# Kernel optimization log

Hardware: AMD Instinct MI355X
Metric: run time of the kernel (lower is better)

## Reference

```python
import jax, jax.numpy as jnp
import numpy as np

B, S, D, H = 1, 4096, 1024, 16
HD = D // H  # 64


def setup_inputs() -> dict:
    key = jax.random.key(0)
    k1, k2, k3, k4, k5 = jax.random.split(key, 5)
    hidden_states = jax.random.normal(k1, (B, S, D), dtype=jnp.float32)
    # rotary frequencies: freqs_cis[s, j] = exp(i * s * theta^(-2j/HD)), stored as (cos, sin)
    inv_freq = 1.0 / (10000.0 ** (jnp.arange(0, HD, 2, dtype=jnp.float32) / HD))  # [HD/2]
    angles = jnp.arange(S, dtype=jnp.float32)[:, None] * inv_freq[None, :]        # [S, HD/2]
    freqs_cis = jnp.stack([jnp.cos(angles), jnp.sin(angles)], axis=-1)            # [S, HD/2, 2]
    attention_mask = jnp.ones((B, S), dtype=jnp.float32)
    scale = 1.0 / np.sqrt(D)
    wq = jax.random.normal(k2, (D, D), dtype=jnp.float32) * scale
    wk = jax.random.normal(k3, (D, D), dtype=jnp.float32) * scale
    wv = jax.random.normal(k4, (D, D), dtype=jnp.float32) * scale
    wo = jax.random.normal(k5, (D, D), dtype=jnp.float32) * scale
    return {"hidden_states": hidden_states, "freqs_cis": freqs_cis,
            "attention_mask": attention_mask, "wq": wq, "wk": wk, "wv": wv, "wo": wo}


def _apply_rope(x, freqs_cis):
    # x: [B, S, H, HD]; freqs_cis: [S, HD/2, 2] (cos, sin)
    b, s, h, hd = x.shape
    xr = x.reshape(b, s, h, hd // 2, 2)
    a, bb = xr[..., 0], xr[..., 1]
    cos = freqs_cis[None, :s, None, :, 0]
    sin = freqs_cis[None, :s, None, :, 1]
    out_r = a * cos - bb * sin
    out_i = a * sin + bb * cos
    return jnp.stack([out_r, out_i], axis=-1).reshape(b, s, h, hd)


def reference(hidden_states, freqs_cis, attention_mask, wq, wk, wv, wo):
    b, s, d = hidden_states.shape
    scaling = HD ** -0.5
    q = (hidden_states @ wq).reshape(b, s, H, HD)
    k = (hidden_states @ wk).reshape(b, s, H, HD)
    v = (hidden_states @ wv).reshape(b, s, H, HD)
    q = _apply_rope(q, freqs_cis)
    k = _apply_rope(k, freqs_cis)
    # [B, H, S, S] scores, exactly as the torch module materializes them
    scores = jnp.einsum('bqhd,bkhd->bhqk', q, k) * scaling
    mask_add = (1.0 - attention_mask)[:, None, None, :] * -10000.0  # [B,1,1,S]
    scores = scores + mask_add
    attn = jax.nn.softmax(scores.astype(jnp.float32), axis=-1).astype(q.dtype)
    out = jnp.einsum('bhqk,bkhd->bqhd', attn, v).reshape(b, s, d)
    return out @ wo
```

## Files before the change

### kernel.cpp

```cpp
#include <hip/hip_runtime.h>
#include <stdint.h>

#define S_LEN 4096
#define DMODEL 1024
#define NH 16
#define HDIM 64
#define LOG2E 1.44269504088896340736f

typedef __attribute__((ext_vector_type(8))) __bf16 bf16x8;
typedef __attribute__((ext_vector_type(4))) __bf16 bf16x4;
typedef __attribute__((ext_vector_type(2))) __bf16 bf16x2;
typedef __attribute__((ext_vector_type(4))) float f32x4;
typedef __attribute__((ext_vector_type(16))) float f32x16;
typedef __attribute__((ext_vector_type(4))) unsigned int uint32x4;

__device__ __forceinline__ void gload_lds16(const __bf16* g, __bf16* l) {
  __builtin_amdgcn_global_load_lds(
      (const __attribute__((address_space(1))) void*)g,
      (__attribute__((address_space(3))) void*)l, 16, 0, 0);
}

__global__ __launch_bounds__(256) void convert_f32_bf16(const float* __restrict__ src,
                                                        __bf16* __restrict__ dst,
                                                        const float* __restrict__ mask,
                                                        float* __restrict__ maskadd) {
  int idx = blockIdx.x * 256 + threadIdx.x;
  f32x4 v = ((const f32x4*)src)[idx];
  bf16x4 o;
#pragma unroll
  for (int i = 0; i < 4; ++i) o[i] = (__bf16)v[i];
  ((bf16x4*)dst)[idx] = o;
  if (idx < S_LEN) maskadd[idx] = (1.0f - mask[idx]) * (-10000.0f * LOG2E);
}

template <typename T>
__global__ __launch_bounds__(256) void transpose_tiles(const T* __restrict__ src,
                                                       __bf16* __restrict__ dst,
                                                       int R, int C) {
  src += (size_t)blockIdx.z * R * C;
  dst += (size_t)blockIdx.z * R * C;
  __shared__ __bf16 tile[64][65];
  const int r0 = blockIdx.y * 64, c0 = blockIdx.x * 64;
  const int t = threadIdx.x;
  const int col = t & 63, rsub = t >> 6;
#pragma unroll
  for (int i = 0; i < 16; ++i) {
    int r = rsub + i * 4;
    tile[r][col] = (__bf16)src[(size_t)(r0 + r) * C + (c0 + col)];
  }
  __syncthreads();
#pragma unroll
  for (int i = 0; i < 16; ++i) {
    int r = rsub + i * 4;
    dst[(size_t)(c0 + r) * R + (r0 + col)] = tile[col][r];
  }
}

template <int EPI>
__global__ __launch_bounds__(256) void gemm_bt(const __bf16* __restrict__ A,
                                               const __bf16* __restrict__ BT,
                                               __bf16* __restrict__ Cq,
                                               __bf16* __restrict__ Ck,
                                               __bf16* __restrict__ Cv,
                                               float* __restrict__ Cout,
                                               int Kdim, int Ndim) {
  __shared__ __align__(16) __bf16 At[128][32];
  __shared__ __align__(16) __bf16 Bt[128][32];
  const int t = threadIdx.x;
  const int wave = t >> 6, lane = t & 63;
  const int wr = wave >> 1, wc = wave & 1;
  const int lrow = lane & 15, lk = lane >> 4;
  const int bm = blockIdx.x, bn = blockIdx.y;

  f32x4 acc[4][4];
#pragma unroll
  for (int i = 0; i < 4; ++i)
#pragma unroll
    for (int j = 0; j < 4; ++j) acc[i][j] = f32x4{0.f, 0.f, 0.f, 0.f};

  const int arow0 = bm * 128, brow0 = bn * 128;
  const int srow = wave * 16 + (lane >> 2);
  const int scol = (lane & 3) * 8;
  const __bf16* gA0 = &A[(size_t)(arow0 + srow) * Kdim + scol];
  const __bf16* gA1 = &A[(size_t)(arow0 + 64 + srow) * Kdim + scol];
  const __bf16* gB0 = &BT[(size_t)(brow0 + srow) * Kdim + scol];
  const __bf16* gB1 = &BT[(size_t)(brow0 + 64 + srow) * Kdim + scol];
  __bf16* lA0 = &At[wave * 16][0];
  __bf16* lA1 = &At[64 + wave * 16][0];
  __bf16* lB0 = &Bt[wave * 16][0];
  __bf16* lB1 = &Bt[64 + wave * 16][0];

  for (int k0 = 0; k0 < Kdim; k0 += 32) {
    __syncthreads();
    gload_lds16(gA0 + k0, lA0);
    gload_lds16(gA1 + k0, lA1);
    gload_lds16(gB0 + k0, lB0);
    gload_lds16(gB1 + k0, lB1);
    __syncthreads();
    bf16x8 af[4], bfr[4];
#pragma unroll
    for (int mi = 0; mi < 4; ++mi)
      af[mi] = *(const bf16x8*)&At[wr * 64 + mi * 16 + lrow][lk * 8];
#pragma unroll
    for (int ni = 0; ni < 4; ++ni)
      bfr[ni] = *(const bf16x8*)&Bt[wc * 64 + ni * 16 + lrow][lk * 8];
#pragma unroll
    for (int mi = 0; mi < 4; ++mi)
#pragma unroll
      for (int ni = 0; ni < 4; ++ni)
        acc[mi][ni] =
            __builtin_amdgcn_mfma_f32_16x16x32_bf16(af[mi], bfr[ni], acc[mi][ni], 0, 0, 0);
  }

  const int rb = bm * 128 + wr * 64 + lk * 4;
  const int cb = bn * 128 + wc * 64 + lrow;
#pragma unroll
  for (int mi = 0; mi < 4; ++mi)
#pragma unroll
    for (int ni = 0; ni < 4; ++ni) {
      int c = cb + ni * 16;
#pragma unroll
      for (int r = 0; r < 4; ++r) {
        int row = rb + mi * 16 + r;
        float v = acc[mi][ni][r];
        if (EPI == 0) {
          Cout[(size_t)row * Ndim + c] = v;
        } else {
          int type = c >> 10, d = c & 1023;
          int hh = d >> 6, hd = d & 63;
          __bf16* dp = (type == 0) ? Cq : (type == 1) ? Ck : Cv;
          dp[((size_t)hh * S_LEN + row) * HDIM + hd] = (__bf16)v;
        }
      }
    }
}

__global__ __launch_bounds__(256) void rope_kernel(__bf16* __restrict__ Q,
                                                   __bf16* __restrict__ Kb,
                                                   const float* __restrict__ freqs) {
  size_t idx = (size_t)blockIdx.x * 256 + threadIdx.x;
  int i = idx & 31;
  size_t rest = idx >> 5;
  int s = rest & 4095;
  int h = (int)(rest >> 12);
  float c = freqs[(s * 32 + i) * 2 + 0];
  float sn = freqs[(s * 32 + i) * 2 + 1];
  size_t base = ((size_t)h * S_LEN + s) * HDIM + 2 * i;
  float qa = (float)Q[base], qb = (float)Q[base + 1];
  Q[base] = (__bf16)(qa * c - qb * sn);
  Q[base + 1] = (__bf16)(qa * sn + qb * c);
  float ka = (float)Kb[base], kb2 = (float)Kb[base + 1];
  Kb[base] = (__bf16)(ka * c - kb2 * sn);
  Kb[base + 1] = (__bf16)(ka * sn + kb2 * c);
}

template <int KS>
__global__ __launch_bounds__(256, 2) void attn_split(const __bf16* __restrict__ Q,
                                                     const __bf16* __restrict__ Kmat,
                                                     const __bf16* __restrict__ Vt,
                                                     const float* __restrict__ maskadd,
                                                     float* __restrict__ Opart,
                                                     float* __restrict__ Lpart) {
  constexpr int KCHUNK = S_LEN / KS;
  __shared__ __align__(16) __bf16 Kl[2][64][64];
  __shared__ __align__(16) __bf16 Vl[2][64][64];

  const int t = threadIdx.x;
  const int id = blockIdx.x;
  const int swz = (id & 7) * (16 * NH * KS / 8) + (id >> 3);
  const int h = swz / (16 * KS);
  const int rem = swz % (16 * KS);
  const int qb = rem / KS;
  const int split = rem % KS;
  const int k0 = split * KCHUNK;
  const int wave = t >> 6, lane = t & 63;
  const int lq = lane & 31, hi = lane >> 5;
  const int sw = lq & 7;

  const __bf16* Kh = Kmat + (size_t)h * S_LEN * HDIM;
  const __bf16* Vh = Vt + (size_t)h * HDIM * S_LEN;

  const int sr = t >> 2;
  const int sc0 = (t & 3) * 2;
  const int scs0 = (sc0 ^ (sr & 7)) * 8;
  const int scs1 = ((sc0 + 1) ^ (sr & 7)) * 8;
  const __bf16* Kgb = Kh + (size_t)sr * HDIM + sc0 * 8;
  const __bf16* Vgb = Vh + (size_t)sr * S_LEN + sc0 * 8;

  uint32x4 kreg0, kreg1, vreg0, vreg1;
  kreg0 = *(const uint32x4*)(Kgb + (size_t)k0 * HDIM);
  kreg1 = *(const uint32x4*)(Kgb + (size_t)k0 * HDIM + 8);
  vreg0 = *(const uint32x4*)(Vgb + k0);
  vreg1 = *(const uint32x4*)(Vgb + k0 + 8);
  *(uint32x4*)&Kl[0][sr][scs0] = kreg0;
  *(uint32x4*)&Kl[0][sr][scs1] = kreg1;
  *(uint32x4*)&Vl[0][sr][scs0] = vreg0;
  *(uint32x4*)&Vl[0][sr][scs1] = vreg1;

  const __bf16* Qh = Q + ((size_t)h * S_LEN + qb * 256 + wave * 64 + lq) * HDIM;
  bf16x8 qfA[4], qfB[4];
#pragma unroll
  for (int ds = 0; ds < 4; ++ds) {
    qfA[ds] = *(const bf16x8*)(Qh + ds * 16 + hi * 8);
    qfB[ds] = *(const bf16x8*)(Qh + (size_t)32 * HDIM + ds * 16 + hi * 8);
  }

  __syncthreads();

  const float SCL = 0.125f * LOG2E;
  float lA = 0.f, lB = 0.f;
  f32x16 oA0, oA1, oB0, oB1;
#pragma unroll
  for (int r = 0; r < 16; ++r) { oA0[r] = 0.f; oA1[r] = 0.f; oB0[r] = 0.f; oB1[r] = 0.f; }

  for (int it = 0; it < KCHUNK / 64; ++it) {
    const int cur = it & 1;
    const int kb = k0 + it * 64;

    if (it < KCHUNK / 64 - 1) {
      kreg0 = *(const uint32x4*)(Kgb + (size_t)(kb + 64) * HDIM);
      kreg1 = *(const uint32x4*)(Kgb + (size_t)(kb + 64) * HDIM + 8);
      vreg0 = *(const uint32x4*)(Vgb + (kb + 64));
      vreg1 = *(const uint32x4*)(Vgb + (kb + 64) + 8);
    }

    f32x16 pA0, pA1, pB0, pB1;
#pragma unroll
    for (int r = 0; r < 16; ++r) { pA0[r] = 0.f; pA1[r] = 0.f; pB0[r] = 0.f; pB1[r] = 0.f; }
    __builtin_amdgcn_s_setprio(1);
#pragma unroll
    for (int ds = 0; ds < 4; ++ds) {
      int sg = ((ds << 1) | hi) ^ sw;
      bf16x8 kf0 = *(const bf16x8*)&Kl[cur][lq][sg * 8];
      pA0 = __builtin_amdgcn_mfma_f32_32x32x16_bf16(kf0, qfA[ds], pA0, 0, 0, 0);
      pB0 = __builtin_amdgcn_mfma_f32_32x32x16_bf16(kf0, qfB[ds], pB0, 0, 0, 0);
    }
#pragma unroll
    for (int ds = 0; ds < 4; ++ds) {
      int sg = ((ds << 1) | hi) ^ sw;
      bf16x8 kf1 = *(const bf16x8*)&Kl[cur][lq + 32][sg * 8];
      pA1 = __builtin_amdgcn_mfma_f32_32x32x16_bf16(kf1, qfA[ds], pA1, 0, 0, 0);
      pB1 = __builtin_amdgcn_mfma_f32_32x32x16_bf16(kf1, qfB[ds], pB1, 0, 0, 0);
    }
    __builtin_amdgcn_s_setprio(0);

#pragma unroll
    for (int tq = 0; tq < 4; ++tq) {
      f32x4 ma0 = *(const f32x4*)&maskadd[kb + tq * 8 + hi * 4];
      f32x4 ma1 = *(const f32x4*)&maskadd[kb + 32 + tq * 8 + hi * 4];
#pragma unroll
      for (int c = 0; c < 4; ++c) {
        pA0[tq * 4 + c] = exp2f(fmaf(pA0[tq * 4 + c], SCL, ma0[c]));
        pB0[tq * 4 + c] = exp2f(fmaf(pB0[tq * 4 + c], SCL, ma0[c]));
        pA1[tq * 4 + c] = exp2f(fmaf(pA1[tq * 4 + c], SCL, ma1[c]));
        pB1[tq * 4 + c] = exp2f(fmaf(pB1[tq * 4 + c], SCL, ma1[c]));
      }
    }
    {
      float a0 = (pA0[0] + pA0[1]) + (pA0[2] + pA0[3]);
      float a1 = (pA0[4] + pA0[5]) + (pA0[6] + pA0[7]);
      float a2 = (pA0[8] + pA0[9]) + (pA0[10] + pA0[11]);
      float a3 = (pA0[12] + pA0[13]) + (pA0[14] + pA0[15]);
      float b0 = (pA1[0] + pA1[1]) + (pA1[2] + pA1[3]);
      float b1 = (pA1[4] + pA1[5]) + (pA1[6] + pA1[7]);
      float b2 = (pA1[8] + pA1[9]) + (pA1[10] + pA1[11]);
      float b3 = (pA1[12] + pA1[13]) + (pA1[14] + pA1[15]);
      float ps = ((a0 + a1) + (a2 + a3)) + ((b0 + b1) + (b2 + b3));
      ps += __shfl_xor(ps, 32);
      lA += ps;
    }
    {
      float a0 = (pB0[0] + pB0[1]) + (pB0[2] + pB0[3]);
      float a1 = (pB0[4] + pB0[5]) + (pB0[6] + pB0[7]);
      float a2 = (pB0[8] + pB0[9]) + (pB0[10] + pB0[11]);
      float a3 = (pB0[12] + pB0[13]) + (pB0[14] + pB0[15]);
      float b0 = (pB1[0] + pB1[1]) + (pB1[2] + pB1[3]);
      float b1 = (pB1[4] + pB1[5]) + (pB1[6] + pB1[7]);
      float b2 = (pB1[8] + pB1[9]) + (pB1[10] + pB1[11]);
      float b3 = (pB1[12] + pB1[13]) + (pB1[14] + pB1[15]);
      float ps = ((a0 + a1) + (a2 + a3)) + ((b0 + b1) + (b2 + b3));
      ps += __shfl_xor(ps, 32);
      lB += ps;
    }

    unsigned int tA0[8], tA1[8], tB0[8], tB1[8];
#pragma unroll
    for (int tp = 0; tp < 8; ++tp) {
      bf16x2 wa0, wa1, wb0, wb1;
      wa0[0] = (__bf16)pA0[2 * tp]; wa0[1] = (__bf16)pA0[2 * tp + 1];
      wa1[0] = (__bf16)pA1[2 * tp]; wa1[1] = (__bf16)pA1[2 * tp + 1];
      wb0[0] = (__bf16)pB0[2 * tp]; wb0[1] = (__bf16)pB0[2 * tp + 1];
      wb1[0] = (__bf16)pB1[2 * tp]; wb1[1] = (__bf16)pB1[2 * tp + 1];
      tA0[tp] = __builtin_bit_cast(unsigned int, wa0);
      tA1[tp] = __builtin_bit_cast(unsigned int, wa1);
      tB0[tp] = __builtin_bit_cast(unsigned int, wb0);
      tB1[tp] = __builtin_bit_cast(unsigned int, wb1);
    }

#pragma unroll
    for (int ks = 0; ks < 4; ++ks) {
      unsigned int a0, a1, a2, a3, b0, b1, b2, b3;
      if (ks == 0)      { a0 = tA0[0]; a1 = tA0[1]; a2 = tA0[2]; a3 = tA0[3];
                          b0 = tB0[0]; b1 = tB0[1]; b2 = tB0[2]; b3 = tB0[3]; }
      else if (ks == 1) { a0 = tA0[4]; a1 = tA0[5]; a2 = tA0[6]; a3 = tA0[7];
                          b0 = tB0[4]; b1 = tB0[5]; b2 = tB0[6]; b3 = tB0[7]; }
      else if (ks == 2) { a0 = tA1[0]; a1 = tA1[1]; a2 = tA1[2]; a3 = tA1[3];
                          b0 = tB1[0]; b1 = tB1[1]; b2 = tB1[2]; b3 = tB1[3]; }
      else              { a0 = tA1[4]; a1 = tA1[5]; a2 = tA1[6]; a3 = tA1[7];
                          b0 = tB1[4]; b1 = tB1[5]; b2 = tB1[6]; b3 = tB1[7]; }
      unsigned int sa0 = hi ? a0 : a2, sa1 = hi ? a1 : a3;
      unsigned int sb0 = hi ? b0 : b2, sb1 = hi ? b1 : b3;
      unsigned int ra0 = (unsigned int)__shfl_xor((int)sa0, 32);
      unsigned int ra1 = (unsigned int)__shfl_xor((int)sa1, 32);
      unsigned int rb0 = (unsigned int)__shfl_xor((int)sb0, 32);
      unsigned int rb1 = (unsigned int)__shfl_xor((int)sb1, 32);
      uint32x4 fa, fb;
      fa[0] = hi ? ra0 : a0; fa[1] = hi ? ra1 : a1;
      fa[2] = hi ? a2 : ra0; fa[3] = hi ? a3 : ra1;
      fb[0] = hi ? rb0 : b0; fb[1] = hi ? rb1 : b1;
      fb[2] = hi ? b2 : rb0; fb[3] = hi ? b3 : rb1;
      bf16x8 fav = __builtin_bit_cast(bf16x8, fa);
      bf16x8 fbv = __builtin_bit_cast(bf16x8, fb);
      int sg = ((ks << 1) | hi) ^ sw;
      bf16x8 v0 = *(const bf16x8*)&Vl[cur][lq][sg * 8];
      bf16x8 v1 = *(const bf16x8*)&Vl[cur][lq + 32][sg * 8];
      __builtin_amdgcn_s_setprio(1);
      oA0 = __builtin_amdgcn_mfma_f32_32x32x16_bf16(v0, fav, oA0, 0, 0, 0);
      oA1 = __builtin_amdgcn_mfma_f32_32x32x16_bf16(v1, fav, oA1, 0, 0, 0);
      oB0 = __builtin_amdgcn_mfma_f32_32x32x16_bf16(v0, fbv, oB0, 0, 0, 0);
      oB1 = __builtin_amdgcn_mfma_f32_32x32x16_bf16(v1, fbv, oB1, 0, 0, 0);
      __builtin_amdgcn_s_setprio(0);
    }

    if (it < KCHUNK / 64 - 1) {
      *(uint32x4*)&Kl[cur ^ 1][sr][scs0] = kreg0;
      *(uint32x4*)&Kl[cur ^ 1][sr][scs1] = kreg1;
      *(uint32x4*)&Vl[cur ^ 1][sr][scs0] = vreg0;
      *(uint32x4*)&Vl[cur ^ 1][sr][scs1] = vreg1;
      __syncthreads();
    }
  }

  const int qrowA = qb * 256 + wave * 64 + lq;
  float* OpA = Opart + (((size_t)split * NH + h) * S_LEN + qrowA) * 64;
  float* OpB = OpA + (size_t)32 * 64;
#pragma unroll
  for (int tq = 0; tq < 4; ++tq) {
    f32x4 a, b, c, d;
#pragma unroll
    for (int cc = 0; cc < 4; ++cc) {
      a[cc] = oA0[tq * 4 + cc]; b[cc] = oA1[tq * 4 + cc];
      c[cc] = oB0[tq * 4 + cc]; d[cc] = oB1[tq * 4 + cc];
    }
    *(f32x4*)(OpA + tq * 8 + hi * 4) = a;
    *(f32x4*)(OpA + 32 + tq * 8 + hi * 4) = b;
    *(f32x4*)(OpB + tq * 8 + hi * 4) = c;
    *(f32x4*)(OpB + 32 + tq * 8 + hi * 4) = d;
  }
  if (hi == 0) {
    Lpart[((size_t)split * NH + h) * S_LEN + qrowA] = lA;
    Lpart[((size_t)split * NH + h) * S_LEN + qrowA + 32] = lB;
  }
}

template <int KS>
__global__ __launch_bounds__(256) void attn_merge(const float* __restrict__ Opart,
                                                  const float* __restrict__ Lpart,
                                                  __bf16* __restrict__ AO) {
  int idx = blockIdx.x * 256 + threadIdx.x;
  int dd = (idx & 15) * 4;
  int hq = idx >> 4;
  int q = hq & (S_LEN - 1), h = hq >> 12;
  float l = 0.f;
  f32x4 acc = f32x4{0.f, 0.f, 0.f, 0.f};
#pragma unroll
  for (int s = 0; s < KS; ++s) {
    l += Lpart[(size_t)s * NH * S_LEN + hq];
    f32x4 a = *(const f32x4*)&Opart[((size_t)s * NH * S_LEN + hq) * 64 + dd];
#pragma unroll
    for (int c = 0; c < 4; ++c) acc[c] += a[c];
  }
  float inv = 1.0f / fmaxf(l, 1e-30f);
  bf16x4 o;
#pragma unroll
  for (int c = 0; c < 4; ++c) o[c] = (__bf16)(acc[c] * inv);
  *(bf16x4*)&AO[(size_t)q * DMODEL + h * HDIM + dd] = o;
}

extern "C" void kernel_launch(void* const* d_in, const int* in_sizes, int n_in,
                              void* d_out, int out_size, void* d_ws, size_t ws_size,
                              hipStream_t stream) {
  const float* X = (const float*)d_in[0];
  const float* freqs = (const float*)d_in[1];
  const float* mask = (const float*)d_in[2];
  const float* wq = (const float*)d_in[3];
  const float* wk = (const float*)d_in[4];
  const float* wv = (const float*)d_in[5];
  const float* wo = (const float*)d_in[6];
  float* out = (float*)d_out;

  __bf16* WTqkv = (__bf16*)d_ws;
  __bf16* WoT = WTqkv + 3072 * 1024;
  __bf16* Xb = WoT + 1024 * 1024;
  __bf16* Qb = Xb + (size_t)S_LEN * DMODEL;
  __bf16* Kb = Qb + (size_t)NH * S_LEN * HDIM;
  __bf16* Vb = Kb + (size_t)NH * S_LEN * HDIM;
  __bf16* Vtb = Vb + (size_t)NH * S_LEN * HDIM;
  __bf16* AO = Vb;

  float* Opart = (float*)(Vtb + (size_t)NH * S_LEN * HDIM);
  float* Lpart = Opart + (size_t)4 * NH * S_LEN * 64;
  float* maskadd = Lpart + (size_t)4 * NH * S_LEN;
  size_t ws_need4 = (size_t)((char*)(maskadd + S_LEN) - (char*)d_ws);

  float* Lpart2 = Opart + (size_t)2 * NH * S_LEN * 64;
  float* maskadd2 = Lpart2 + (size_t)2 * NH * S_LEN;

  const bool use4 = (ws_size >= ws_need4);
  float* Lp = use4 ? Lpart : Lpart2;
  float* ma = use4 ? maskadd : maskadd2;

  convert_f32_bf16<<<dim3(S_LEN * DMODEL / 1024), 256, 0, stream>>>(X, Xb, mask, ma);

  transpose_tiles<float><<<dim3(16, 16, 1), 256, 0, stream>>>(wq, WTqkv, 1024, 1024);
  transpose_tiles<float><<<dim3(16, 16, 1), 256, 0, stream>>>(wk, WTqkv + 1024 * 1024, 1024, 1024);
  transpose_tiles<float><<<dim3(16, 16, 1), 256, 0, stream>>>(wv, WTqkv + 2 * 1024 * 1024, 1024, 1024);
  transpose_tiles<float><<<dim3(16, 16, 1), 256, 0, stream>>>(wo, WoT, 1024, 1024);

  gemm_bt<1><<<dim3(32, 24), 256, 0, stream>>>(Xb, WTqkv, Qb, Kb, Vb, nullptr, 1024, 3072);

  rope_kernel<<<dim3((NH * S_LEN * 32) / 256), 256, 0, stream>>>(Qb, Kb, freqs);

  transpose_tiles<__bf16><<<dim3(1, 64, NH), 256, 0, stream>>>(Vb, Vtb, S_LEN, HDIM);

  if (use4) {
    attn_split<4><<<dim3(16 * NH * 4), 256, 0, stream>>>(Qb, Kb, Vtb, ma, Opart, Lp);
    attn_merge<4><<<dim3(NH * S_LEN * 16 / 256), 256, 0, stream>>>(Opart, Lp, AO);
  } else {
    attn_split<2><<<dim3(16 * NH * 2), 256, 0, stream>>>(Qb, Kb, Vtb, ma, Opart, Lp);
    attn_merge<2><<<dim3(NH * S_LEN * 16 / 256), 256, 0, stream>>>(Opart, Lp, AO);
  }

  gemm_bt<0><<<dim3(32, 8), 256, 0, stream>>>(AO, WoT, nullptr, nullptr, nullptr, out, 1024, 1024);
}
```

Before: 221.9 us.

## Use direct global-to-LDS loads, 3-way KV split, and half-tile softmax in attention

The attention kernel now stages K/V tiles with global_load_lds (async direct-to-LDS) instead of loading into registers and then storing to shared memory. The score tile is processed in two 32-column halves to cut live registers, and launch bounds go from 2 to 3 blocks per CU. The KV split drops from 4 to 3 chunks, with uneven 22/21/21 tile counts, to fit 768 blocks onto the CUs. The row-sum shuffle moves out of the loop. Risks are lower per-block parallelism from fewer splits, and register spills under the tighter occupancy bound.

```diff
diff --git a/kernel.cpp b/kernel.cpp
--- a/kernel.cpp
+++ b/kernel.cpp
@@ -155,47 +155,51 @@
 }
 
 template <int KS>
-__global__ __launch_bounds__(256, 2) void attn_split(const __bf16* __restrict__ Q,
+__global__ __launch_bounds__(256, 3) void attn_split(const __bf16* __restrict__ Q,
                                                      const __bf16* __restrict__ Kmat,
                                                      const __bf16* __restrict__ Vt,
                                                      const float* __restrict__ maskadd,
                                                      float* __restrict__ Opart,
                                                      float* __restrict__ Lpart) {
-  constexpr int KCHUNK = S_LEN / KS;
   __shared__ __align__(16) __bf16 Kl[2][64][64];
   __shared__ __align__(16) __bf16 Vl[2][64][64];
 
   const int t = threadIdx.x;
   const int id = blockIdx.x;
-  const int swz = (id & 7) * (16 * NH * KS / 8) + (id >> 3);
+  const int swz = (id & 7) * (32 * KS) + (id >> 3);
   const int h = swz / (16 * KS);
   const int rem = swz % (16 * KS);
   const int qb = rem / KS;
   const int split = rem % KS;
-  const int k0 = split * KCHUNK;
   const int wave = t >> 6, lane = t & 63;
   const int lq = lane & 31, hi = lane >> 5;
   const int sw = lq & 7;
 
+  int it0, nt;
+  if constexpr (KS == 3) {
+    it0 = split * 21 + (split > 0 ? 1 : 0);
+    nt = (split == 0) ? 22 : 21;
+  } else {
+    it0 = split * (64 / KS);
+    nt = 64 / KS;
+  }
+
   const __bf16* Kh = Kmat + (size_t)h * S_LEN * HDIM;
   const __bf16* Vh = Vt + (size_t)h * HDIM * S_LEN;
 
-  const int sr = t >> 2;
-  const int sc0 = (t & 3) * 2;
-  const int scs0 = (sc0 ^ (sr & 7)) * 8;
-  const int scs1 = ((sc0 + 1) ^ (sr & 7)) * 8;
-  const __bf16* Kgb = Kh + (size_t)sr * HDIM + sc0 * 8;
-  const __bf16* Vgb = Vh + (size_t)sr * S_LEN + sc0 * 8;
-
-  uint32x4 kreg0, kreg1, vreg0, vreg1;
-  kreg0 = *(const uint32x4*)(Kgb + (size_t)k0 * HDIM);
-  kreg1 = *(const uint32x4*)(Kgb + (size_t)k0 * HDIM + 8);
-  vreg0 = *(const uint32x4*)(Vgb + k0);
-  vreg1 = *(const uint32x4*)(Vgb + k0 + 8);
-  *(uint32x4*)&Kl[0][sr][scs0] = kreg0;
-  *(uint32x4*)&Kl[0][sr][scs1] = kreg1;
-  *(uint32x4*)&Vl[0][sr][scs0] = vreg0;
-  *(uint32x4*)&Vl[0][sr][scs1] = vreg1;
+  const int rofs = lane >> 3;
+  const int seg = (lane & 7) ^ rofs;
+  const __bf16* Kg0 = Kh + (size_t)(wave * 16 + rofs) * HDIM + seg * 8;
+  const __bf16* Vg0 = Vh + (size_t)(wave * 16 + rofs) * S_LEN + seg * 8;
+  const __bf16* Vg1 = Vh + (size_t)(wave * 16 + 8 + rofs) * S_LEN + seg * 8;
+
+  {
+    const int kb0 = it0 * 64;
+    gload_lds16(Kg0 + (size_t)kb0 * HDIM, &Kl[0][wave * 16][0]);
+    gload_lds16(Kg0 + (size_t)kb0 * HDIM + 8 * HDIM, &Kl[0][wave * 16 + 8][0]);
+    gload_lds16(Vg0 + kb0, &Vl[0][wave * 16][0]);
+    gload_lds16(Vg1 + kb0, &Vl[0][wave * 16 + 8][0]);
+  }
 
   const __bf16* Qh = Q + ((size_t)h * S_LEN + qb * 256 + wave * 64 + lq) * HDIM;
   bf16x8 qfA[4], qfB[4];
@@ -208,139 +212,103 @@
   __syncthreads();
 
   const float SCL = 0.125f * LOG2E;
-  float lA = 0.f, lB = 0.f;
+  float sA = 0.f, sB = 0.f;
   f32x16 oA0, oA1, oB0, oB1;
 #pragma unroll
   for (int r = 0; r < 16; ++r) { oA0[r] = 0.f; oA1[r] = 0.f; oB0[r] = 0.f; oB1[r] = 0.f; }
 
-  for (int it = 0; it < KCHUNK / 64; ++it) {
+  for (int it = 0; it < nt; ++it) {
     const int cur = it & 1;
-    const int kb = k0 + it * 64;
-
-    if (it < KCHUNK / 64 - 1) {
-      kreg0 = *(const uint32x4*)(Kgb + (size_t)(kb + 64) * HDIM);
-      kreg1 = *(const uint32x4*)(Kgb + (size_t)(kb + 64) * HDIM + 8);
-      vreg0 = *(const uint32x4*)(Vgb + (kb + 64));
-      vreg1 = *(const uint32x4*)(Vgb + (kb + 64) + 8);
+    const int kb = (it0 + it) * 64;
+
+    if (it < nt - 1) {
+      const int kn = kb + 64;
+      gload_lds16(Kg0 + (size_t)kn * HDIM, &Kl[cur ^ 1][wave * 16][0]);
+      gload_lds16(Kg0 + (size_t)kn * HDIM + 8 * HDIM, &Kl[cur ^ 1][wave * 16 + 8][0]);
+      gload_lds16(Vg0 + kn, &Vl[cur ^ 1][wave * 16][0]);
+      gload_lds16(Vg1 + kn, &Vl[cur ^ 1][wave * 16 + 8][0]);
     }
 
-    f32x16 pA0, pA1, pB0, pB1;
-#pragma unroll
-    for (int r = 0; r < 16; ++r) { pA0[r] = 0.f; pA1[r] = 0.f; pB0[r] = 0.f; pB1[r] = 0.f; }
-    __builtin_amdgcn_s_setprio(1);
-#pragma unroll
-    for (int ds = 0; ds < 4; ++ds) {
-      int sg = ((ds << 1) | hi) ^ sw;
-      bf16x8 kf0 = *(const bf16x8*)&Kl[cur][lq][sg * 8];
-      pA0 = __builtin_amdgcn_mfma_f32_32x32x16_bf16(kf0, qfA[ds], pA0, 0, 0, 0);
-      pB0 = __builtin_amdgcn_mfma_f32_32x32x16_bf16(kf0, qfB[ds], pB0, 0, 0, 0);
-    }
-#pragma unroll
-    for (int ds = 0; ds < 4; ++ds) {
-      int sg = ((ds << 1) | hi) ^ sw;
-      bf16x8 kf1 = *(const bf16x8*)&Kl[cur][lq + 32][sg * 8];
-      pA1 = __builtin_amdgcn_mfma_f32_32x32x16_bf16(kf1, qfA[ds], pA1, 0, 0, 0);
-      pB1 = __builtin_amdgcn_mfma_f32_32x32x16_bf16(kf1, qfB[ds], pB1, 0, 0, 0);
-    }
-    __builtin_amdgcn_s_setprio(0);
-
-#pragma unroll
-    for (int tq = 0; tq < 4; ++tq) {
-      f32x4 ma0 = *(const f32x4*)&maskadd[kb + tq * 8 + hi * 4];
-      f32x4 ma1 = *(const f32x4*)&maskadd[kb + 32 + tq * 8 + hi * 4];
-#pragma unroll
-      for (int c = 0; c < 4; ++c) {
-        pA0[tq * 4 + c] = exp2f(fmaf(pA0[tq * 4 + c], SCL, ma0[c]));
-        pB0[tq * 4 + c] = exp2f(fmaf(pB0[tq * 4 + c], SCL, ma0[c]));
-        pA1[tq * 4 + c] = exp2f(fmaf(pA1[tq * 4 + c], SCL, ma1[c]));
-        pB1[tq * 4 + c] = exp2f(fmaf(pB1[tq * 4 + c], SCL, ma1[c]));
+#pragma unroll
+    for (int half = 0; half < 2; ++half) {
+      const int krow = half * 32 + lq;
+      f32x16 pA, pB;
+#pragma unroll
+      for (int r = 0; r < 16; ++r) { pA[r] = 0.f; pB[r] = 0.f; }
+      __builtin_amdgcn_s_setprio(1);
+#pragma unroll
+      for (int ds = 0; ds < 4; ++ds) {
+        int sg = ((ds << 1) | hi) ^ sw;
+        bf16x8 kf = *(const bf16x8*)&Kl[cur][krow][sg * 8];
+        pA = __builtin_amdgcn_mfma_f32_32x32x16_bf16(kf, qfA[ds], pA, 0, 0, 0);
+        pB = __builtin_amdgcn_mfma_f32_32x32x16_bf16(kf, qfB[ds], pB, 0, 0, 0);
+      }
+      __builtin_amdgcn_s_setprio(0);
+
+#pragma unroll
+      for (int tq = 0; tq < 4; ++tq) {
+        f32x4 ma = *(const f32x4*)&maskadd[kb + half * 32 + tq * 8 + hi * 4];
+#pragma unroll
+        for (int c = 0; c < 4; ++c) {
+          pA[tq * 4 + c] = exp2f(fmaf(pA[tq * 4 + c], SCL, ma[c]));
+          pB[tq * 4 + c] = exp2f(fmaf(pB[tq * 4 + c], SCL, ma[c]));
+        }
+      }
+      {
+        float a0 = (pA[0] + pA[1]) + (pA[2] + pA[3]);
+        float a1 = (pA[4] + pA[5]) + (pA[6] + pA[7]);
+        float a2 = (pA[8] + pA[9]) + (pA[10] + pA[11]);
+        float a3 = (pA[12] + pA[13]) + (pA[14] + pA[15]);
+        sA += (a0 + a1) + (a2 + a3);
+        float b0 = (pB[0] + pB[1]) + (pB[2] + pB[3]);
+        float b1 = (pB[4] + pB[5]) + (pB[6] + pB[7]);
+        float b2 = (pB[8] + pB[9]) + (pB[10] + pB[11]);
+        float b3 = (pB[12] + pB[13]) + (pB[14] + pB[15]);
+        sB += (b0 + b1) + (b2 + b3);
+      }
+
+#pragma unroll
+      for (int ksq = 0; ksq < 2; ++ksq) {
+        unsigned int aq[4], bq[4];
+#pragma unroll
+        for (int j = 0; j < 4; ++j) {
+          bf16x2 wa, wb;
+          wa[0] = (__bf16)pA[8 * ksq + 2 * j]; wa[1] = (__bf16)pA[8 * ksq + 2 * j + 1];
+          wb[0] = (__bf16)pB[8 * ksq + 2 * j]; wb[1] = (__bf16)pB[8 * ksq + 2 * j + 1];
+          aq[j] = __builtin_bit_cast(unsigned int, wa);
+          bq[j] = __builtin_bit_cast(unsigned int, wb);
+        }
+        unsigned int sa0 = hi ? aq[0] : aq[2], sa1 = hi ? aq[1] : aq[3];
+        unsigned int sb0 = hi ? bq[0] : bq[2], sb1 = hi ? bq[1] : bq[3];
+        unsigned int ra0 = (unsigned int)__shfl_xor((int)sa0, 32);
+        unsigned int ra1 = (unsigned int)__shfl_xor((int)sa1, 32);
+        unsigned int rb0 = (unsigned int)__shfl_xor((int)sb0, 32);
+        unsigned int rb1 = (unsigned int)__shfl_xor((int)sb1, 32);
+        uint32x4 fa, fb;
+        fa[0] = hi ? ra0 : aq[0]; fa[1] = hi ? ra1 : aq[1];
+        fa[2] = hi ? aq[2] : ra0; fa[3] = hi ? aq[3] : ra1;
+        fb[0] = hi ? rb0 : bq[0]; fb[1] = hi ? rb1 : bq[1];
+        fb[2] = hi ? bq[2] : rb0; fb[3] = hi ? bq[3] : rb1;
+        bf16x8 fav = __builtin_bit_cast(bf16x8, fa);
+        bf16x8 fbv = __builtin_bit_cast(bf16x8, fb);
+        const int ks = half * 2 + ksq;
+        int sg = ((ks << 1) | hi) ^ sw;
+        bf16x8 v0 = *(const bf16x8*)&Vl[cur][lq][sg * 8];
+        bf16x8 v1 = *(const bf16x8*)&Vl[cur][lq + 32][sg * 8];
+        __builtin_amdgcn_s_setprio(1);
+        oA0 = __builtin_amdgcn_mfma_f32_32x32x16_bf16(v0, fav, oA0, 0, 0, 0);
+        oA1 = __builtin_amdgcn_mfma_f32_32x32x16_bf16(v1, fav, oA1, 0, 0, 0);
+        oB0 = __builtin_amdgcn_mfma_f32_32x32x16_bf16(v0, fbv, oB0, 0, 0, 0);
+        oB1 = __builtin_amdgcn_mfma_f32_32x32x16_bf16(v1, fbv, oB1, 0, 0, 0);
+        __builtin_amdgcn_s_setprio(0);
       }
     }
-    {
-      float a0 = (pA0[0] + pA0[1]) + (pA0[2] + pA0[3]);
-      float a1 = (pA0[4] + pA0[5]) + (pA0[6] + pA0[7]);
-      float a2 = (pA0[8] + pA0[9]) + (pA0[10] + pA0[11]);
-      float a3 = (pA0[12] + pA0[13]) + (pA0[14] + pA0[15]);
-      float b0 = (pA1[0] + pA1[1]) + (pA1[2] + pA1[3]);
-      float b1 = (pA1[4] + pA1[5]) + (pA1[6] + pA1[7]);
-      float b2 = (pA1[8] + pA1[9]) + (pA1[10] + pA1[11]);
-      float b3 = (pA1[12] + pA1[13]) + (pA1[14] + pA1[15]);
-      float ps = ((a0 + a1) + (a2 + a3)) + ((b0 + b1) + (b2 + b3));
-      ps += __shfl_xor(ps, 32);
-      lA += ps;
-    }
-    {
-      float a0 = (pB0[0] + pB0[1]) + (pB0[2] + pB0[3]);
-      float a1 = (pB0[4] + pB0[5]) + (pB0[6] + pB0[7]);
-      float a2 = (pB0[8] + pB0[9]) + (pB0[10] + pB0[11]);
-      float a3 = (pB0[12] + pB0[13]) + (pB0[14] + pB0[15]);
-      float b0 = (pB1[0] + pB1[1]) + (pB1[2] + pB1[3]);
-      float b1 = (pB1[4] + pB1[5]) + (pB1[6] + pB1[7]);
-      float b2 = (pB1[8] + pB1[9]) + (pB1[10] + pB1[11]);
-      float b3 = (pB1[12] + pB1[13]) + (pB1[14] + pB1[15]);
-      float ps = ((a0 + a1) + (a2 + a3)) + ((b0 + b1) + (b2 + b3));
-      ps += __shfl_xor(ps, 32);
-      lB += ps;
-    }
-
-    unsigned int tA0[8], tA1[8], tB0[8], tB1[8];
-#pragma unroll
-    for (int tp = 0; tp < 8; ++tp) {
-      bf16x2 wa0, wa1, wb0, wb1;
-      wa0[0] = (__bf16)pA0[2 * tp]; wa0[1] = (__bf16)pA0[2 * tp + 1];
-      wa1[0] = (__bf16)pA1[2 * tp]; wa1[1] = (__bf16)pA1[2 * tp + 1];
-      wb0[0] = (__bf16)pB0[2 * tp]; wb0[1] = (__bf16)pB0[2 * tp + 1];
-      wb1[0] = (__bf16)pB1[2 * tp]; wb1[1] = (__bf16)pB1[2 * tp + 1];
-      tA0[tp] = __builtin_bit_cast(unsigned int, wa0);
-      tA1[tp] = __builtin_bit_cast(unsigned int, wa1);
-      tB0[tp] = __builtin_bit_cast(unsigned int, wb0);
-      tB1[tp] = __builtin_bit_cast(unsigned int, wb1);
-    }
-
-#pragma unroll
-    for (int ks = 0; ks < 4; ++ks) {
-      unsigned int a0, a1, a2, a3, b0, b1, b2, b3;
-      if (ks == 0)      { a0 = tA0[0]; a1 = tA0[1]; a2 = tA0[2]; a3 = tA0[3];
-                          b0 = tB0[0]; b1 = tB0[1]; b2 = tB0[2]; b3 = tB0[3]; }
-      else if (ks == 1) { a0 = tA0[4]; a1 = tA0[5]; a2 = tA0[6]; a3 = tA0[7];
-                          b0 = tB0[4]; b1 = tB0[5]; b2 = tB0[6]; b3 = tB0[7]; }
-      else if (ks == 2) { a0 = tA1[0]; a1 = tA1[1]; a2 = tA1[2]; a3 = tA1[3];
-                          b0 = tB1[0]; b1 = tB1[1]; b2 = tB1[2]; b3 = tB1[3]; }
-      else              { a0 = tA1[4]; a1 = tA1[5]; a2 = tA1[6]; a3 = tA1[7];
-                          b0 = tB1[4]; b1 = tB1[5]; b2 = tB1[6]; b3 = tB1[7]; }
-      unsigned int sa0 = hi ? a0 : a2, sa1 = hi ? a1 : a3;
-      unsigned int sb0 = hi ? b0 : b2, sb1 = hi ? b1 : b3;
-      unsigned int ra0 = (unsigned int)__shfl_xor((int)sa0, 32);
-      unsigned int ra1 = (unsigned int)__shfl_xor((int)sa1, 32);
-      unsigned int rb0 = (unsigned int)__shfl_xor((int)sb0, 32);
-      unsigned int rb1 = (unsigned int)__shfl_xor((int)sb1, 32);
-      uint32x4 fa, fb;
-      fa[0] = hi ? ra0 : a0; fa[1] = hi ? ra1 : a1;
-      fa[2] = hi ? a2 : ra0; fa[3] = hi ? a3 : ra1;
-      fb[0] = hi ? rb0 : b0; fb[1] = hi ? rb1 : b1;
-      fb[2] = hi ? b2 : rb0; fb[3] = hi ? b3 : rb1;
-      bf16x8 fav = __builtin_bit_cast(bf16x8, fa);
-      bf16x8 fbv = __builtin_bit_cast(bf16x8, fb);
-      int sg = ((ks << 1) | hi) ^ sw;
-      bf16x8 v0 = *(const bf16x8*)&Vl[cur][lq][sg * 8];
-      bf16x8 v1 = *(const bf16x8*)&Vl[cur][lq + 32][sg * 8];
-      __builtin_amdgcn_s_setprio(1);
-      oA0 = __builtin_amdgcn_mfma_f32_32x32x16_bf16(v0, fav, oA0, 0, 0, 0);
-      oA1 = __builtin_amdgcn_mfma_f32_32x32x16_bf16(v1, fav, oA1, 0, 0, 0);
-      oB0 = __builtin_amdgcn_mfma_f32_32x32x16_bf16(v0, fbv, oB0, 0, 0, 0);
-      oB1 = __builtin_amdgcn_mfma_f32_32x32x16_bf16(v1, fbv, oB1, 0, 0, 0);
-      __builtin_amdgcn_s_setprio(0);
-    }
-
-    if (it < KCHUNK / 64 - 1) {
-      *(uint32x4*)&Kl[cur ^ 1][sr][scs0] = kreg0;
-      *(uint32x4*)&Kl[cur ^ 1][sr][scs1] = kreg1;
-      *(uint32x4*)&Vl[cur ^ 1][sr][scs0] = vreg0;
-      *(uint32x4*)&Vl[cur ^ 1][sr][scs1] = vreg1;
-      __syncthreads();
-    }
-  }
-
+
+    if (it < nt - 1) __syncthreads();
+  }
+
+  float lA = sA + __shfl_xor(sA, 32);
+  float lB = sB + __shfl_xor(sB, 32);
   const int qrowA = qb * 256 + wave * 64 + lq;
   float* OpA = Opart + (((size_t)split * NH + h) * S_LEN + qrowA) * 64;
   float* OpB = OpA + (size_t)32 * 64;
@@ -409,16 +377,16 @@
   __bf16* AO = Vb;
 
   float* Opart = (float*)(Vtb + (size_t)NH * S_LEN * HDIM);
-  float* Lpart = Opart + (size_t)4 * NH * S_LEN * 64;
-  float* maskadd = Lpart + (size_t)4 * NH * S_LEN;
-  size_t ws_need4 = (size_t)((char*)(maskadd + S_LEN) - (char*)d_ws);
+  float* Lpart3 = Opart + (size_t)3 * NH * S_LEN * 64;
+  float* maskadd3 = Lpart3 + (size_t)3 * NH * S_LEN;
+  size_t ws_need3 = (size_t)((char*)(maskadd3 + S_LEN) - (char*)d_ws);
 
   float* Lpart2 = Opart + (size_t)2 * NH * S_LEN * 64;
   float* maskadd2 = Lpart2 + (size_t)2 * NH * S_LEN;
 
-  const bool use4 = (ws_size >= ws_need4);
-  float* Lp = use4 ? Lpart : Lpart2;
-  float* ma = use4 ? maskadd : maskadd2;
+  const bool use3 = (ws_size >= ws_need3);
+  float* Lp = use3 ? Lpart3 : Lpart2;
+  float* ma = use3 ? maskadd3 : maskadd2;
 
   convert_f32_bf16<<<dim3(S_LEN * DMODEL / 1024), 256, 0, stream>>>(X, Xb, mask, ma);
 
@@ -433,11 +401,11 @@
 
   transpose_tiles<__bf16><<<dim3(1, 64, NH), 256, 0, stream>>>(Vb, Vtb, S_LEN, HDIM);
 
-  if (use4) {
-    attn_split<4><<<dim3(16 * NH * 4), 256, 0, stream>>>(Qb, Kb, Vtb, ma, Opart, Lp);
-    attn_merge<4><<<dim3(NH * S_LEN * 16 / 256), 256, 0, stream>>>(Opart, Lp, AO);
+  if (use3) {
+    attn_split<3><<<dim3(256 * 3), 256, 0, stream>>>(Qb, Kb, Vtb, ma, Opart, Lp);
+    attn_merge<3><<<dim3(NH * S_LEN * 16 / 256), 256, 0, stream>>>(Opart, Lp, AO);
   } else {
-    attn_split<2><<<dim3(16 * NH * 2), 256, 0, stream>>>(Qb, Kb, Vtb, ma, Opart, Lp);
+    attn_split<2><<<dim3(256 * 2), 256, 0, stream>>>(Qb, Kb, Vtb, ma, Opart, Lp);
     attn_merge<2><<<dim3(NH * S_LEN * 16 / 256), 256, 0, stream>>>(Opart, Lp, AO);
   }
 
```

New measurement: 271.0 us. 22.1% more time.

## Fuse RoPE and V transpose into QKV GEMM epilogue, fix split to 2

Applied to the files above, without the earlier changes.

The QKV projection epilogue now applies rotary embedding to Q and K, using a lane shuffle to fetch the paired element, and writes V directly in transposed head-major layout. This removes the separate rope kernel and the V transpose kernel, along with their global memory round trips. The attention key-split is fixed at 2 instead of choosing 4 when workspace allows, which lowers partial-result traffic but reduces grid parallelism. The transposed V stores are strided 8-byte writes, which may coalesce poorly.

```diff
diff --git a/kernel.cpp b/kernel.cpp
--- a/kernel.cpp
+++ b/kernel.cpp
@@ -5,11 +5,14 @@
 #define DMODEL 1024
 #define NH 16
 #define HDIM 64
+#define KSPLIT 2
+#define KCHUNK (S_LEN / KSPLIT)
 #define LOG2E 1.44269504088896340736f
 
 typedef __attribute__((ext_vector_type(8))) __bf16 bf16x8;
 typedef __attribute__((ext_vector_type(4))) __bf16 bf16x4;
 typedef __attribute__((ext_vector_type(2))) __bf16 bf16x2;
+typedef __attribute__((ext_vector_type(2))) float f32x2;
 typedef __attribute__((ext_vector_type(4))) float f32x4;
 typedef __attribute__((ext_vector_type(16))) float f32x16;
 typedef __attribute__((ext_vector_type(4))) unsigned int uint32x4;
@@ -61,7 +64,8 @@
                                                const __bf16* __restrict__ BT,
                                                __bf16* __restrict__ Cq,
                                                __bf16* __restrict__ Ck,
-                                               __bf16* __restrict__ Cv,
+                                               __bf16* __restrict__ Cvt,
+                                               const float* __restrict__ freqs,
                                                float* __restrict__ Cout,
                                                int Kdim, int Ndim) {
   __shared__ __align__(16) __bf16 At[128][32];
@@ -119,39 +123,35 @@
 #pragma unroll
     for (int ni = 0; ni < 4; ++ni) {
       int c = cb + ni * 16;
-#pragma unroll
-      for (int r = 0; r < 4; ++r) {
-        int row = rb + mi * 16 + r;
-        float v = acc[mi][ni][r];
-        if (EPI == 0) {
-          Cout[(size_t)row * Ndim + c] = v;
+      if (EPI == 0) {
+#pragma unroll
+        for (int r = 0; r < 4; ++r)
+          Cout[(size_t)(rb + mi * 16 + r) * Ndim + c] = acc[mi][ni][r];
+      } else {
+        const int type = c >> 10;
+        const int d = c & 1023;
+        const int hh = d >> 6, hd = d & 63;
+        if (type == 2) {
+          bf16x4 pk;
+#pragma unroll
+          for (int r = 0; r < 4; ++r) pk[r] = (__bf16)acc[mi][ni][r];
+          *(bf16x4*)&Cvt[((size_t)hh * HDIM + hd) * S_LEN + rb + mi * 16] = pk;
         } else {
-          int type = c >> 10, d = c & 1023;
-          int hh = d >> 6, hd = d & 63;
-          __bf16* dp = (type == 0) ? Cq : (type == 1) ? Ck : Cv;
-          dp[((size_t)hh * S_LEN + row) * HDIM + hd] = (__bf16)v;
+          __bf16* dp = (type == 0) ? Cq : Ck;
+          const int i = hd >> 1;
+          const float sgn = (hd & 1) ? 1.0f : -1.0f;
+#pragma unroll
+          for (int r = 0; r < 4; ++r) {
+            int row = rb + mi * 16 + r;
+            float v = acc[mi][ni][r];
+            float w = __shfl_xor(v, 1);
+            f32x2 cs = *(const f32x2*)&freqs[((size_t)row * 32 + i) * 2];
+            float out = fmaf(v, cs[0], sgn * w * cs[1]);
+            dp[((size_t)hh * S_LEN + row) * HDIM + hd] = (__bf16)out;
+          }
         }
       }
     }
-}
-
-__global__ __launch_bounds__(256) void rope_kernel(__bf16* __restrict__ Q,
-                                                   __bf16* __restrict__ Kb,
-                                                   const float* __restrict__ freqs) {
-  size_t idx = (size_t)blockIdx.x * 256 + threadIdx.x;
-  int i = idx & 31;
-  size_t rest = idx >> 5;
-  int s = rest & 4095;
-  int h = (int)(rest >> 12);
-  float c = freqs[(s * 32 + i) * 2 + 0];
-  float sn = freqs[(s * 32 + i) * 2 + 1];
-  size_t base = ((size_t)h * S_LEN + s) * HDIM + 2 * i;
-  float qa = (float)Q[base], qb = (float)Q[base + 1];
-  Q[base] = (__bf16)(qa * c - qb * sn);
-  Q[base + 1] = (__bf16)(qa * sn + qb * c);
-  float ka = (float)Kb[base], kb2 = (float)Kb[base + 1];
-  Kb[base] = (__bf16)(ka * c - kb2 * sn);
-  Kb[base + 1] = (__bf16)(ka * sn + kb2 * c);
 }
 
 template <int KS>
@@ -161,7 +161,7 @@
                                                      const float* __restrict__ maskadd,
                                                      float* __restrict__ Opart,
                                                      float* __restrict__ Lpart) {
-  constexpr int KCHUNK = S_LEN / KS;
+  constexpr int KC = S_LEN / KS;
   __shared__ __align__(16) __bf16 Kl[2][64][64];
   __shared__ __align__(16) __bf16 Vl[2][64][64];
 
@@ -172,7 +172,7 @@
   const int rem = swz % (16 * KS);
   const int qb = rem / KS;
   const int split = rem % KS;
-  const int k0 = split * KCHUNK;
+  const int k0 = split * KC;
   const int wave = t >> 6, lane = t & 63;
   const int lq = lane & 31, hi = lane >> 5;
   const int sw = lq & 7;
@@ -213,11 +213,11 @@
 #pragma unroll
   for (int r = 0; r < 16; ++r) { oA0[r] = 0.f; oA1[r] = 0.f; oB0[r] = 0.f; oB1[r] = 0.f; }
 
-  for (int it = 0; it < KCHUNK / 64; ++it) {
+  for (int it = 0; it < KC / 64; ++it) {
     const int cur = it & 1;
     const int kb = k0 + it * 64;
 
-    if (it < KCHUNK / 64 - 1) {
+    if (it < KC / 64 - 1) {
       kreg0 = *(const uint32x4*)(Kgb + (size_t)(kb + 64) * HDIM);
       kreg1 = *(const uint32x4*)(Kgb + (size_t)(kb + 64) * HDIM + 8);
       vreg0 = *(const uint32x4*)(Vgb + (kb + 64));
@@ -332,7 +332,7 @@
       __builtin_amdgcn_s_setprio(0);
     }
 
-    if (it < KCHUNK / 64 - 1) {
+    if (it < KC / 64 - 1) {
       *(uint32x4*)&Kl[cur ^ 1][sr][scs0] = kreg0;
       *(uint32x4*)&Kl[cur ^ 1][sr][scs1] = kreg1;
       *(uint32x4*)&Vl[cur ^ 1][sr][scs0] = vreg0;
@@ -404,42 +404,24 @@
   __bf16* Xb = WoT + 1024 * 1024;
   __bf16* Qb = Xb + (size_t)S_LEN * DMODEL;
   __bf16* Kb = Qb + (size_t)NH * S_LEN * HDIM;
-  __bf16* Vb = Kb + (size_t)NH * S_LEN * HDIM;
-  __bf16* Vtb = Vb + (size_t)NH * S_LEN * HDIM;
-  __bf16* AO = Vb;
-
-  float* Opart = (float*)(Vtb + (size_t)NH * S_LEN * HDIM);
-  float* Lpart = Opart + (size_t)4 * NH * S_LEN * 64;
-  float* maskadd = Lpart + (size_t)4 * NH * S_LEN;
-  size_t ws_need4 = (size_t)((char*)(maskadd + S_LEN) - (char*)d_ws);
-
-  float* Lpart2 = Opart + (size_t)2 * NH * S_LEN * 64;
-  float* maskadd2 = Lpart2 + (size_t)2 * NH * S_LEN;
-
-  const bool use4 = (ws_size >= ws_need4);
-  float* Lp = use4 ? Lpart : Lpart2;
-  float* ma = use4 ? maskadd : maskadd2;
-
-  convert_f32_bf16<<<dim3(S_LEN * DMODEL / 1024), 256, 0, stream>>>(X, Xb, mask, ma);
+  __bf16* Vtb = Kb + (size_t)NH * S_LEN * HDIM;
+  __bf16* AO = Vtb + (size_t)NH * S_LEN * HDIM;
+
+  float* Opart = (float*)(AO + (size_t)S_LEN * DMODEL);
+  float* Lpart = Opart + (size_t)KSPLIT * NH * S_LEN * 64;
+  float* maskadd = Lpart + (size_t)KSPLIT * NH * S_LEN;
+
+  convert_f32_bf16<<<dim3(S_LEN * DMODEL / 1024), 256, 0, stream>>>(X, Xb, mask, maskadd);
 
   transpose_tiles<float><<<dim3(16, 16, 1), 256, 0, stream>>>(wq, WTqkv, 1024, 1024);
   transpose_tiles<float><<<dim3(16, 16, 1), 256, 0, stream>>>(wk, WTqkv + 1024 * 1024, 1024, 1024);
   transpose_tiles<float><<<dim3(16, 16, 1), 256, 0, stream>>>(wv, WTqkv + 2 * 1024 * 1024, 1024, 1024);
   transpose_tiles<float><<<dim3(16, 16, 1), 256, 0, stream>>>(wo, WoT, 1024, 1024);
 
-  gemm_bt<1><<<dim3(32, 24), 256, 0, stream>>>(Xb, WTqkv, Qb, Kb, Vb, nullptr, 1024, 3072);
-
-  rope_kernel<<<dim3((NH * S_LEN * 32) / 256), 256, 0, stream>>>(Qb, Kb, freqs);
-
-  transpose_tiles<__bf16><<<dim3(1, 64, NH), 256, 0, stream>>>(Vb, Vtb, S_LEN, HDIM);
-
-  if (use4) {
-    attn_split<4><<<dim3(16 * NH * 4), 256, 0, stream>>>(Qb, Kb, Vtb, ma, Opart, Lp);
-    attn_merge<4><<<dim3(NH * S_LEN * 16 / 256), 256, 0, stream>>>(Opart, Lp, AO);
-  } else {
-    attn_split<2><<<dim3(16 * NH * 2), 256, 0, stream>>>(Qb, Kb, Vtb, ma, Opart, Lp);
-    attn_merge<2><<<dim3(NH * S_LEN * 16 / 256), 256, 0, stream>>>(Opart, Lp, AO);
-  }
-
-  gemm_bt<0><<<dim3(32, 8), 256, 0, stream>>>(AO, WoT, nullptr, nullptr, nullptr, out, 1024, 1024);
-}
+  gemm_bt<1><<<dim3(32, 24), 256, 0, stream>>>(Xb, WTqkv, Qb, Kb, Vtb, freqs, nullptr, 1024, 3072);
+
+  attn_split<KSPLIT><<<dim3(16 * NH * KSPLIT), 256, 0, stream>>>(Qb, Kb, Vtb, maskadd, Opart, Lpart);
+  attn_merge<KSPLIT><<<dim3(NH * S_LEN * 16 / 256), 256, 0, stream>>>(Opart, Lpart, AO);
+
+  gemm_bt<0><<<dim3(32, 8), 256, 0, stream>>>(AO, WoT, nullptr, nullptr, nullptr, nullptr, out, 1024, 1024);
+}
```

Result: faster. 204.9 us (-7.6%).
